# Performance work log

Hardware: AMD Instinct MI355X
Metric: run time of the kernel (lower is better)

The kernel has to match this reference:

```python
import jax, jax.numpy as jnp
import numpy as np

EPS = 1e-6
NUM_HEADS = 16

def layernorm(x, alpha, bias):
    # Faithful to the torch module: torch.std uses ddof=1, and eps is added to std.
    mean = jnp.mean(x, axis=-1, keepdims=True)
    std = jnp.std(x, axis=-1, keepdims=True, ddof=1)
    return alpha * (x - mean) / (std + EPS) + bias

def setup_inputs() -> dict:
    key = jax.random.key(0)
    B, S, D, F = 4, 2048, 1024, 4096
    ks = jax.random.split(key, 8)
    s = 1.0 / np.sqrt(D)
    inp = {
        'x': jax.random.normal(ks[0], (B, S, D), jnp.float32),
        'src_mask': jnp.ones((B, 1, 1, S), jnp.int32),
        'wq': jax.random.normal(ks[1], (D, D), jnp.float32) * s,
        'bq': jnp.zeros((D,), jnp.float32),
        'wk': jax.random.normal(ks[2], (D, D), jnp.float32) * s,
        'bk': jnp.zeros((D,), jnp.float32),
        'wv': jax.random.normal(ks[3], (D, D), jnp.float32) * s,
        'bv': jnp.zeros((D,), jnp.float32),
        'wo': jax.random.normal(ks[4], (D, D), jnp.float32) * s,
        'bo': jnp.zeros((D,), jnp.float32),
        'w1': jax.random.normal(ks[5], (D, F), jnp.float32) * s,
        'b1': jnp.zeros((F,), jnp.float32),
        'w2': jax.random.normal(ks[6], (F, D), jnp.float32) * (1.0 / np.sqrt(F)),
        'b2': jnp.zeros((D,), jnp.float32),
        'ln1_a': jnp.ones((D,), jnp.float32),
        'ln1_b': jnp.zeros((D,), jnp.float32),
        'ln2_a': jnp.ones((D,), jnp.float32),
        'ln2_b': jnp.zeros((D,), jnp.float32),
    }
    return inp

def mha(x, src_mask, wq, bq, wk, bk, wv, bv, wo, bo):
    B, S, D = x.shape
    H = NUM_HEADS
    dk = D // H
    q = (x @ wq + bq).reshape(B, S, H, dk).transpose(0, 2, 1, 3)  # [B,H,S,dk]
    k = (x @ wk + bk).reshape(B, S, H, dk).transpose(0, 2, 1, 3)
    v = (x @ wv + bv).reshape(B, S, H, dk).transpose(0, 2, 1, 3)
    scores = jnp.einsum('bhqd,bhkd->bhqk', q, k) / np.sqrt(dk)  # [B,H,S,S]
    scores = jnp.where(src_mask == 0, -1e9, scores)
    p = jax.nn.softmax(scores, axis=-1)
    ctx = jnp.einsum('bhqk,bhkd->bhqd', p, v)  # [B,H,S,dk]
    ctx = ctx.transpose(0, 2, 1, 3).reshape(B, S, D)
    return ctx @ wo + bo

def reference(x, src_mask, wq, bq, wk, bk, wv, bv, wo, bo,
              w1, b1, w2, b2, ln1_a, ln1_b, ln2_a, ln2_b):
    # residual 1: pre-norm self-attention (dropout is identity in eval)
    h = x + mha(layernorm(x, ln1_a, ln1_b), src_mask, wq, bq, wk, bk, wv, bv, wo, bo)
    # residual 2: pre-norm FFN
    hn = layernorm(h, ln2_a, ln2_b)
    ffn = jax.nn.relu(hn @ w1 + b1) @ w2 + b2
    return h + ffn
```

## Files before the change

### kernel.cpp

```cpp
#include <hip/hip_runtime.h>
#include <hip/hip_bf16.h>

typedef __attribute__((ext_vector_type(8))) short bf16x8;
typedef __attribute__((ext_vector_type(4))) short bf16x4;
typedef __attribute__((ext_vector_type(4))) float f32x4;
typedef __hip_bfloat16 bf16;
typedef unsigned short u16;

#define B_ 4
#define S_ 2048
#define D_ 1024
#define F_ 4096
#define H_ 16
#define MROWS 8192
#define QSCALE 0.18033688011116012f

__device__ __forceinline__ unsigned pkbf(float lo, float hi){
  union{float f; unsigned u;} a, b; a.f = lo; b.f = hi;
  return __builtin_amdgcn_perm(b.u + 0x8000u, a.u + 0x8000u, 0x07060302);
}
__device__ __forceinline__ u16 bfrnd(float f){
  union{float ff; unsigned u;} c; c.ff = f;
  return (u16)((c.u + 0x8000u) >> 16);
}
__device__ __forceinline__ void gll16(const bf16* gp, u16* lp){
  __builtin_amdgcn_global_load_lds(
      (const __attribute__((address_space(1))) void*)gp,
      (__attribute__((address_space(3))) void*)lp, 16, 0, 0);
}

struct PrepArgs { const float* w[6]; const float* b[3]; };
__global__ __launch_bounds__(256) void prep(
    PrepArgs pa, bf16* __restrict__ wqkvoT, bf16* __restrict__ w1T,
    bf16* __restrict__ w2T, float* __restrict__ bqkv)
{
  __shared__ float tl[32][33];
  const int bid = blockIdx.x, tid = threadIdx.x;
  const int x = tid&31, y = tid>>5;
  if (bid < 12288) {
    const float* W; bf16* dst; int K, N, nb, kb;
    if (bid < 4096)      { int wi=bid>>10, t=bid&1023; W=pa.w[wi]; dst=wqkvoT+(size_t)wi*1048576; K=1024; N=1024; nb=t&31;  kb=t>>5; }
    else if (bid < 8192) { int t=bid-4096;             W=pa.w[4];  dst=w1T;  K=1024; N=4096; nb=t&127; kb=t>>7; }
    else                 { int t=bid-8192;             W=pa.w[5];  dst=w2T;  K=4096; N=1024; nb=t&31;  kb=t>>5; }
    const int n0=nb*32, k0=kb*32;
    #pragma unroll
    for (int i=0;i<32;i+=8)
      tl[y+i][x] = W[(size_t)(k0+y+i)*N + n0+x];
    __syncthreads();
    #pragma unroll
    for (int i=0;i<32;i+=8)
      dst[(size_t)(n0+y+i)*K + k0+x] = __float2bfloat16(tl[x][y+i]);
  } else {
    for (int i=tid; i<3072; i+=256) bqkv[i] = pa.b[i>>10][i&1023];
  }
}

__global__ __launch_bounds__(256) void v_transpose(
    const bf16* __restrict__ qkv, bf16* __restrict__ vT)
{
  __shared__ u16 tile[64*65];
  const int bh = blockIdx.y, b = bh>>4, h = bh&15;
  const int s0 = blockIdx.x*64;
  const int tid = threadIdx.x;
  const bf16* src = qkv + (size_t)(b*S_ + s0)*3072 + 2048 + h*64;
  #pragma unroll
  for (int i=0;i<2;i++){
    int idx = i*256 + tid;
    int r = idx>>3, sg = idx&7;
    uint4 v = *reinterpret_cast<const uint4*>(src + (size_t)r*3072 + sg*8);
    const u16* e = (const u16*)&v;
    #pragma unroll
    for (int j=0;j<8;j++) tile[r*65 + sg*8 + j] = e[j];
  }
  __syncthreads();
  bf16* dst = vT + (size_t)bh*64*S_ + s0;
  #pragma unroll
  for (int i=0;i<2;i++){
    int idx = i*256 + tid;
    int d = idx>>3, sg = idx&7;
    u16 tmp[8];
    #pragma unroll
    for (int j=0;j<8;j++) tmp[j] = tile[(sg*8+j)*65 + d];
    *reinterpret_cast<uint4*>(dst + (size_t)d*S_ + sg*8) = *reinterpret_cast<uint4*>(tmp);
  }
}

__device__ __forceinline__ float block_reduce_256(float v, float* sbuf){
  #pragma unroll
  for (int o=32;o>0;o>>=1) v += __shfl_down(v, o);
  int wave = threadIdx.x>>6;
  if ((threadIdx.x&63)==0) sbuf[wave] = v;
  __syncthreads();
  float r = sbuf[0]+sbuf[1]+sbuf[2]+sbuf[3];
  __syncthreads();
  return r;
}

__global__ __launch_bounds__(256) void ln_fwd(
    const float* __restrict__ x, const float* __restrict__ alpha,
    const float* __restrict__ beta, bf16* __restrict__ out)
{
  __shared__ float sbuf[4];
  int row = blockIdx.x, tid = threadIdx.x;
  const float4* xr = reinterpret_cast<const float4*>(x + (size_t)row*D_);
  float4 v = xr[tid];
  float sum = block_reduce_256(v.x+v.y+v.z+v.w, sbuf);
  float mean = sum * (1.0f/1024.0f);
  float dx0=v.x-mean, dx1=v.y-mean, dx2=v.z-mean, dx3=v.w-mean;
  float ssq = block_reduce_256(dx0*dx0+dx1*dx1+dx2*dx2+dx3*dx3, sbuf);
  float std_ = sqrtf(ssq * (1.0f/1023.0f));
  float inv = 1.0f/(std_ + 1e-6f);
  const float4* ar = reinterpret_cast<const float4*>(alpha);
  const float4* br = reinterpret_cast<const float4*>(beta);
  float4 a = ar[tid], bb = br[tid];
  unsigned* o = reinterpret_cast<unsigned*>(out + (size_t)row*D_);
  o[tid*2+0] = pkbf(a.x*dx0*inv + bb.x, a.y*dx1*inv + bb.y);
  o[tid*2+1] = pkbf(a.z*dx2*inv + bb.z, a.w*dx3*inv + bb.w);
}

template<int EPI>
__global__ __launch_bounds__(512) void gemm_bt(
    const bf16* __restrict__ A, const bf16* __restrict__ BT,
    const float* __restrict__ bias, const float* __restrict__ res,
    void* __restrict__ out, int M, int N, int K)
{
  __shared__ __align__(16) u16 As[128*32];
  __shared__ __align__(16) u16 Bs[128*32];
  const int tid = threadIdx.x;
  const int m0 = blockIdx.x*128, n0 = blockIdx.y*128;
  const int wave = tid>>6, lane = tid&63;
  const int wm = (wave>>2)*64, wn = (wave&3)*32;
  const int lrow = lane&15, quad = lane>>4;
  const int srow = wave*16 + (lane>>2);
  const int sseg = lane&3;
  const bf16* apg = A  + (size_t)(m0+srow)*K + sseg*8;
  const bf16* bpg = BT + (size_t)(n0+srow)*K + sseg*8;
  u16* asd = &As[wave*512];
  u16* bsd = &Bs[wave*512];

  f32x4 acc[4][2];
  #pragma unroll
  for (int i=0;i<4;i++)
    #pragma unroll
    for (int j=0;j<2;j++) acc[i][j] = (f32x4){0.f,0.f,0.f,0.f};

  for (int k0=0; k0<K; k0+=32) {
    gll16(apg + k0, asd);
    gll16(bpg + k0, bsd);
    __syncthreads();
    bf16x8 a[4], b[2];
    #pragma unroll
    for (int t=0;t<4;t++)
      a[t] = *reinterpret_cast<const bf16x8*>(&As[(wm + t*16 + lrow)*32 + quad*8]);
    #pragma unroll
    for (int t=0;t<2;t++)
      b[t] = *reinterpret_cast<const bf16x8*>(&Bs[(wn + t*16 + lrow)*32 + quad*8]);
    #pragma unroll
    for (int mt=0;mt<4;mt++)
      #pragma unroll
      for (int nt=0;nt<2;nt++)
        acc[mt][nt] = __builtin_amdgcn_mfma_f32_16x16x32_bf16(a[mt], b[nt], acc[mt][nt], 0,0,0);
    __syncthreads();
  }

  #pragma unroll
  for (int mt=0;mt<4;mt++){
    #pragma unroll
    for (int nt=0;nt<2;nt++){
      int col = n0 + wn + nt*16 + lrow;
      float bv = bias[col];
      float sc = (EPI == 3 && col < 1024) ? QSCALE : 1.0f;
      #pragma unroll
      for (int r=0;r<4;r++){
        int row = m0 + wm + mt*16 + quad*4 + r;
        size_t idx = (size_t)row*N + col;
        float val = acc[mt][nt][r] + bv;
        if (EPI == 1) val = fmaxf(val, 0.0f);
        if (EPI == 3) val *= sc;
        if (EPI == 2) {
          ((float*)out)[idx] = val + res[idx];
        } else {
          ((u16*)out)[idx] = bfrnd(val);
        }
      }
    }
  }
}

#define KP 72

__global__ __launch_bounds__(512) void flash_attn_mfma(
    const bf16* __restrict__ qkv, const bf16* __restrict__ vT,
    const int* __restrict__ mask, bf16* __restrict__ ctx)
{
  __shared__ __align__(16) u16 Ks[64*KP];
  __shared__ __align__(16) u16 Vt[64*KP];
  __shared__ __align__(16) float Mb[64];

  const int b = blockIdx.z, h = blockIdx.y, qt = blockIdx.x;
  const int tid = threadIdx.x, wave = tid>>6, lane = tid&63;
  const int lr = lane&15, quad = lane>>4;
  const int qbase = qt*256 + wave*32;

  const bf16* base = qkv + (size_t)b*S_*3072 + h*64;
  const bf16* vtb  = vT + (size_t)(b*H_+h)*64*S_;
  const int*  mrow = mask + b*S_;

  bf16x8 qf[2][2];
  #pragma unroll
  for (int c=0;c<2;c++){
    const bf16* qp = base + (size_t)(qbase + c*16 + lr)*3072 + quad*8;
    qf[c][0] = *reinterpret_cast<const bf16x8*>(qp);
    qf[c][1] = *reinterpret_cast<const bf16x8*>(qp + 32);
  }

  const bf16x4 ones4 = {(short)0x3F80,(short)0x3F80,(short)0x3F80,(short)0x3F80};

  f32x4 actx[2][4];
  f32x4 acc_l[2];
  #pragma unroll
  for (int c=0;c<2;c++){
    #pragma unroll
    for (int dt=0;dt<4;dt++) actx[c][dt] = (f32x4){0.f,0.f,0.f,0.f};
    acc_l[c] = (f32x4){0.f,0.f,0.f,0.f};
  }

  const int sr = tid>>3, sg = tid&7;

  for (int kt=0; kt<S_; kt+=64){
    *reinterpret_cast<uint4*>(&Ks[sr*KP + sg*8]) =
      *reinterpret_cast<const uint4*>(base + 1024 + (size_t)(kt+sr)*3072 + sg*8);
    *reinterpret_cast<uint4*>(&Vt[sr*KP + sg*8]) =
      *reinterpret_cast<const uint4*>(vtb + (size_t)sr*S_ + kt + sg*8);
    if (tid < 64) Mb[tid] = (mrow[kt+tid]==0) ? -2e9f : 0.0f;
    unsigned long long bal = __ballot(mrow[kt + lane] == 0);
    __syncthreads();

    bf16x4 pk[2][4];
    if (bal == 0ULL) {
      #pragma unroll
      for (int nt=0;nt<4;nt++){
        bf16x8 kf0 = *reinterpret_cast<const bf16x8*>(&Ks[(nt*16+lr)*KP + quad*8]);
        bf16x8 kf1 = *reinterpret_cast<const bf16x8*>(&Ks[(nt*16+lr)*KP + 32 + quad*8]);
        #pragma unroll
        for (int c=0;c<2;c++){
          f32x4 a = (f32x4){0.f,0.f,0.f,0.f};
          a = __builtin_amdgcn_mfma_f32_16x16x32_bf16(kf0, qf[c][0], a, 0,0,0);
          a = __builtin_amdgcn_mfma_f32_16x16x32_bf16(kf1, qf[c][1], a, 0,0,0);
          uint2 w;
          w.x = pkbf(__builtin_amdgcn_exp2f(a[0]), __builtin_amdgcn_exp2f(a[1]));
          w.y = pkbf(__builtin_amdgcn_exp2f(a[2]), __builtin_amdgcn_exp2f(a[3]));
          union{uint2 u; bf16x4 v;} cvt; cvt.u = w;
          pk[c][nt] = cvt.v;
        }
      }
    } else {
      #pragma unroll
      for (int nt=0;nt<4;nt++){
        bf16x8 kf0 = *reinterpret_cast<const bf16x8*>(&Ks[(nt*16+lr)*KP + quad*8]);
        bf16x8 kf1 = *reinterpret_cast<const bf16x8*>(&Ks[(nt*16+lr)*KP + 32 + quad*8]);
        float4 mb = *reinterpret_cast<const float4*>(&Mb[nt*16 + quad*4]);
        #pragma unroll
        for (int c=0;c<2;c++){
          f32x4 a = (f32x4){0.f,0.f,0.f,0.f};
          a = __builtin_amdgcn_mfma_f32_16x16x32_bf16(kf0, qf[c][0], a, 0,0,0);
          a = __builtin_amdgcn_mfma_f32_16x16x32_bf16(kf1, qf[c][1], a, 0,0,0);
          uint2 w;
          w.x = pkbf(__builtin_amdgcn_exp2f(a[0]+mb.x), __builtin_amdgcn_exp2f(a[1]+mb.y));
          w.y = pkbf(__builtin_amdgcn_exp2f(a[2]+mb.z), __builtin_amdgcn_exp2f(a[3]+mb.w));
          union{uint2 u; bf16x4 v;} cvt; cvt.u = w;
          pk[c][nt] = cvt.v;
        }
      }
    }

    #pragma unroll
    for (int dt=0;dt<4;dt++){
      #pragma unroll
      for (int kc=0;kc<4;kc++){
        bf16x4 vf = *reinterpret_cast<const bf16x4*>(&Vt[(dt*16+lr)*KP + kc*16 + quad*4]);
        #pragma unroll
        for (int c=0;c<2;c++)
          actx[c][dt] = __builtin_amdgcn_mfma_f32_16x16x16bf16_1k(vf, pk[c][kc], actx[c][dt], 0,0,0);
      }
    }
    #pragma unroll
    for (int kc=0;kc<4;kc++)
      #pragma unroll
      for (int c=0;c<2;c++)
        acc_l[c] = __builtin_amdgcn_mfma_f32_16x16x16bf16_1k(ones4, pk[c][kc], acc_l[c], 0,0,0);
    __syncthreads();
  }

  #pragma unroll
  for (int c=0;c<2;c++){
    float inv = 1.0f/acc_l[c][0];
    int q = qbase + c*16 + lr;
    bf16* op = ctx + (size_t)(b*S_+q)*D_ + h*64 + quad*4;
    #pragma unroll
    for (int dt=0;dt<4;dt++){
      uint2 o;
      o.x = pkbf(actx[c][dt][0]*inv, actx[c][dt][1]*inv);
      o.y = pkbf(actx[c][dt][2]*inv, actx[c][dt][3]*inv);
      *reinterpret_cast<uint2*>(op + dt*16) = o;
    }
  }
}

extern "C" void kernel_launch(void* const* d_in, const int* in_sizes, int n_in,
                              void* d_out, int out_size, void* d_ws, size_t ws_size,
                              hipStream_t stream) {
  const float* x    = (const float*)d_in[0];
  const int*   mask = (const int*)  d_in[1];
  const float* wq   = (const float*)d_in[2];
  const float* bq   = (const float*)d_in[3];
  const float* wk   = (const float*)d_in[4];
  const float* bk   = (const float*)d_in[5];
  const float* wv   = (const float*)d_in[6];
  const float* bv   = (const float*)d_in[7];
  const float* wo   = (const float*)d_in[8];
  const float* bo   = (const float*)d_in[9];
  const float* w1   = (const float*)d_in[10];
  const float* b1   = (const float*)d_in[11];
  const float* w2   = (const float*)d_in[12];
  const float* b2   = (const float*)d_in[13];
  const float* ln1a = (const float*)d_in[14];
  const float* ln1b = (const float*)d_in[15];
  const float* ln2a = (const float*)d_in[16];
  const float* ln2b = (const float*)d_in[17];

  char* ws = (char*)d_ws;
  bf16*  wqkvT = (bf16*) (ws + 0);
  bf16*  woT   = (bf16*) (ws + 6291456);
  bf16*  w1T   = (bf16*) (ws + 8388608);
  bf16*  w2T   = (bf16*) (ws + 16777216);
  float* bqkv  = (float*)(ws + 25165824);
  bf16*  xn    = (bf16*) (ws + 25178112);
  bf16*  vT    = (bf16*) (ws + 25178112);
  bf16*  qkv   = (bf16*) (ws + 41955328);
  bf16*  ctx   = (bf16*) (ws + 92286976);
  bf16*  hn    = (bf16*) (ws + 109064192);
  bf16*  act   = (bf16*) (ws + 25178112);

  PrepArgs pa;
  pa.w[0]=wq; pa.w[1]=wk; pa.w[2]=wv; pa.w[3]=wo; pa.w[4]=w1; pa.w[5]=w2;
  pa.b[0]=bq; pa.b[1]=bk; pa.b[2]=bv;
  prep<<<12289,256,0,stream>>>(pa, wqkvT, w1T, w2T, bqkv);

  ln_fwd<<<8192,256,0,stream>>>(x, ln1a, ln1b, xn);
  gemm_bt<3><<<dim3(64,24),512,0,stream>>>(xn, wqkvT, bqkv, nullptr, qkv, MROWS,3072,1024);
  v_transpose<<<dim3(32,64),256,0,stream>>>(qkv, vT);
  flash_attn_mfma<<<dim3(S_/256,H_,B_),512,0,stream>>>(qkv, vT, mask, ctx);
  gemm_bt<2><<<dim3(64,8),512,0,stream>>>(ctx, woT, bo, x, d_out, MROWS,1024,1024);
  ln_fwd<<<8192,256,0,stream>>>((const float*)d_out, ln2a, ln2b, hn);
  gemm_bt<1><<<dim3(64,32),512,0,stream>>>(hn, w1T, b1, nullptr, act, MROWS,F_,1024);
  gemm_bt<2><<<dim3(64,8),512,0,stream>>>(act, w2T, b2, (const float*)d_out, d_out, MROWS,1024,F_);
}
```

Baseline: 549.0 us.

## Add 256x256-tile pipelined GEMM kernel for QKV and FFN1 projections

Adds a new GEMM kernel with 256x256 output tiles, 128KB of dynamic LDS, XOR-swizzled fragment loads and direct global-to-LDS staging. Each K-step is split into four phases that interleave staging of the next tiles with MFMA work, using barriers and setprio. An XCD-aware block swizzle is also applied. It replaces the older gemm_bt for the QKV and W1 projections to raise data reuse and overlap memory with compute. The cost is higher register and LDS pressure, which lowers occupancy, and a harder schedule that falls back to the old kernel if the LDS attribute call fails.

```diff
diff --git a/kernel.cpp b/kernel.cpp
--- a/kernel.cpp
+++ b/kernel.cpp
@@ -182,6 +182,128 @@
         } else {
           ((u16*)out)[idx] = bfrnd(val);
         }
+      }
+    }
+  }
+}
+
+#define LA256(bu,hf) (lds + (((bu)*2+0)*2+(hf))*8192)
+#define LB256(bu,hf) (lds + (((bu)*2+1)*2+(hf))*8192)
+
+__device__ __forceinline__ bf16x8 ldfrag(const u16* base, int row, int chunk){
+  int pc = chunk ^ (row & 7);
+  return *reinterpret_cast<const bf16x8*>(base + row*64 + pc*8);
+}
+
+__device__ __forceinline__ void stage_half256(const bf16* __restrict__ src, int K,
+                                              u16* lbase, int wave, int lane){
+  #pragma unroll
+  for (int i=0;i<2;i++){
+    int q = i*512 + wave*64 + lane;
+    int row = q>>3;
+    int seg = (q&7) ^ (row&7);
+    gll16(src + (size_t)row*K + seg*8, lbase + (i*512 + wave*64)*8);
+  }
+}
+
+template<int RH, int KS, bool RB, typename STG, typename TAIL>
+__device__ __forceinline__ void gphase(const u16* pa, const u16* pb, int bcol,
+    int lr, int quad, bf16x8 (&b)[4][2], f32x4 (&acc)[8][4], STG stg, TAIL tail)
+{
+  bf16x8 a_[4];
+  #pragma unroll
+  for (int ar=0; ar<4; ar++)
+    a_[ar] = ldfrag(pa, RH*64 + ar*16 + lr, KS*4 + quad);
+  if constexpr (RB){
+    #pragma unroll
+    for (int cb=0; cb<4; cb++){
+      b[cb][0] = ldfrag(pb, bcol + cb*16 + lr, quad);
+      b[cb][1] = ldfrag(pb, bcol + cb*16 + lr, 4 + quad);
+    }
+  }
+  stg();
+  __builtin_amdgcn_s_barrier();
+  asm volatile("s_waitcnt lgkmcnt(0)" ::: "memory");
+  __builtin_amdgcn_sched_barrier(0);
+  __builtin_amdgcn_s_setprio(1);
+  #pragma unroll
+  for (int ar=0; ar<4; ar++)
+    #pragma unroll
+    for (int cb=0; cb<4; cb++)
+      acc[RH*4+ar][cb] = __builtin_amdgcn_mfma_f32_16x16x32_bf16(a_[ar], b[cb][KS], acc[RH*4+ar][cb], 0,0,0);
+  __builtin_amdgcn_s_setprio(0);
+  tail();
+  __builtin_amdgcn_s_barrier();
+}
+
+template<int EPI>
+__global__ __launch_bounds__(512,2) void gemm256(
+    const bf16* __restrict__ A, const bf16* __restrict__ BT,
+    const float* __restrict__ bias, bf16* __restrict__ out, int N, int K)
+{
+  extern __shared__ __align__(16) u16 lds[];
+  const int tid = threadIdx.x, wave = tid>>6, lane = tid&63;
+  const int wr = wave>>2, wc = wave&3;
+  const int lr = lane&15, quad = lane>>4;
+  const int gx = gridDim.x;
+  const int nwg = gx*gridDim.y;
+  int flat = blockIdx.y*gx + blockIdx.x;
+  int cpx = nwg>>3;
+  int swz = (flat&7)*cpx + (flat>>3);
+  const int m0 = (swz % gx)*256, n0 = (swz / gx)*256;
+  const int T = K>>6;
+
+  const bf16* Ag = A  + (size_t)m0*K;
+  const bf16* Bg = BT + (size_t)n0*K;
+  const int bcol = (wc&1)*64;
+
+  f32x4 acc[8][4];
+  #pragma unroll
+  for (int i=0;i<8;i++)
+    #pragma unroll
+    for (int j=0;j<4;j++) acc[i][j] = (f32x4){0.f,0.f,0.f,0.f};
+
+  stage_half256(Ag,                       K, LA256(0,0), wave, lane);
+  stage_half256(Ag + (size_t)128*K,       K, LA256(0,1), wave, lane);
+  stage_half256(Bg,                       K, LB256(0,0), wave, lane);
+  stage_half256(Bg + (size_t)128*K,       K, LB256(0,1), wave, lane);
+  stage_half256(Bg + 64,                  K, LB256(1,0), wave, lane);
+  stage_half256(Bg + (size_t)128*K + 64,  K, LB256(1,1), wave, lane);
+  asm volatile("s_waitcnt vmcnt(4)" ::: "memory");
+  __builtin_amdgcn_s_barrier();
+
+  for (int t=0; t<T; ++t){
+    const int bu = t&1, nbu = bu^1;
+    const u16* pa = LA256(bu, wr);
+    const u16* pb = LB256(bu, wc>>1);
+    const size_t ktA = (size_t)((t+1 < T) ? t+1 : T-1)*64;
+    const size_t ktB = (size_t)((t+2 < T) ? t+2 : T-1)*64;
+    bf16x8 b[4][2];
+    gphase<0,0,true >(pa, pb, bcol, lr, quad, b, acc,
+        [&]{ stage_half256(Ag + ktA,                 K, LA256(nbu,0), wave, lane); }, [&]{});
+    gphase<1,0,false>(pa, pb, bcol, lr, quad, b, acc,
+        [&]{ stage_half256(Ag + (size_t)128*K + ktA, K, LA256(nbu,1), wave, lane); }, [&]{});
+    gphase<0,1,false>(pa, pb, bcol, lr, quad, b, acc,
+        [&]{ stage_half256(Bg + ktB,                 K, LB256(bu,0),  wave, lane); }, [&]{});
+    gphase<1,1,false>(pa, pb, bcol, lr, quad, b, acc,
+        [&]{ stage_half256(Bg + (size_t)128*K + ktB, K, LB256(bu,1),  wave, lane); },
+        [&]{ asm volatile("s_waitcnt vmcnt(4)" ::: "memory"); });
+  }
+
+  #pragma unroll
+  for (int mi=0; mi<8; mi++){
+    const int row0 = m0 + wr*128 + (mi>>2)*64 + (mi&3)*16 + quad*4;
+    #pragma unroll
+    for (int cb=0; cb<4; cb++){
+      const int col = n0 + wc*64 + cb*16 + lr;
+      float bv = bias[col];
+      float sc = (EPI==3 && col < 1024) ? QSCALE : 1.0f;
+      #pragma unroll
+      for (int r=0; r<4; r++){
+        float val = acc[mi][cb][r] + bv;
+        if (EPI == 1) val = fmaxf(val, 0.0f);
+        if (EPI == 3) val *= sc;
+        ((u16*)out)[(size_t)(row0+r)*N + col] = bfrnd(val);
       }
     }
   }
@@ -342,17 +464,31 @@
   bf16*  hn    = (bf16*) (ws + 109064192);
   bf16*  act   = (bf16*) (ws + 25178112);
 
+  static bool newgemm_ok = [](){
+    hipError_t e1 = hipFuncSetAttribute((const void*)gemm256<3>,
+        hipFuncAttributeMaxDynamicSharedMemorySize, 131072);
+    hipError_t e2 = hipFuncSetAttribute((const void*)gemm256<1>,
+        hipFuncAttributeMaxDynamicSharedMemorySize, 131072);
+    return e1 == hipSuccess && e2 == hipSuccess;
+  }();
+
   PrepArgs pa;
   pa.w[0]=wq; pa.w[1]=wk; pa.w[2]=wv; pa.w[3]=wo; pa.w[4]=w1; pa.w[5]=w2;
   pa.b[0]=bq; pa.b[1]=bk; pa.b[2]=bv;
   prep<<<12289,256,0,stream>>>(pa, wqkvT, w1T, w2T, bqkv);
 
   ln_fwd<<<8192,256,0,stream>>>(x, ln1a, ln1b, xn);
-  gemm_bt<3><<<dim3(64,24),512,0,stream>>>(xn, wqkvT, bqkv, nullptr, qkv, MROWS,3072,1024);
+  if (newgemm_ok)
+    gemm256<3><<<dim3(32,12),512,131072,stream>>>(xn, wqkvT, bqkv, qkv, 3072, 1024);
+  else
+    gemm_bt<3><<<dim3(64,24),512,0,stream>>>(xn, wqkvT, bqkv, nullptr, qkv, MROWS,3072,1024);
   v_transpose<<<dim3(32,64),256,0,stream>>>(qkv, vT);
   flash_attn_mfma<<<dim3(S_/256,H_,B_),512,0,stream>>>(qkv, vT, mask, ctx);
   gemm_bt<2><<<dim3(64,8),512,0,stream>>>(ctx, woT, bo, x, d_out, MROWS,1024,1024);
   ln_fwd<<<8192,256,0,stream>>>((const float*)d_out, ln2a, ln2b, hn);
-  gemm_bt<1><<<dim3(64,32),512,0,stream>>>(hn, w1T, b1, nullptr, act, MROWS,F_,1024);
+  if (newgemm_ok)
+    gemm256<1><<<dim3(32,16),512,131072,stream>>>(hn, w1T, b1, act, F_, 1024);
+  else
+    gemm_bt<1><<<dim3(64,32),512,0,stream>>>(hn, w1T, b1, nullptr, act, MROWS,F_,1024);
   gemm_bt<2><<<dim3(64,8),512,0,stream>>>(act, w2T, b2, (const float*)d_out, d_out, MROWS,1024,F_);
 }
```

Measured after the change: 547.1 us. Within noise of the previous version (-0.4%).
